# Optimization experiments

Measured on AMD Instinct MI355X. Metric: run time of the kernel, lower is better.

The kernel has to match this reference:

```python
import jax, jax.numpy as jnp
import numpy as np

G, B, I, H = 512, 64, 32, 64  # num_of_grids, batch, input_size, hidden_size


def setup_inputs() -> dict:
    key = jax.random.key(0)
    ks = jax.random.split(key, 13)
    s = lambda *sh: 1.0 / np.sqrt(sh[-1])
    return {
        "input_data": jax.random.normal(ks[0], (G, B, I), jnp.float32),
        "h0": jax.random.normal(ks[1], (B, H), jnp.float32),
        "c0": jax.random.normal(ks[2], (B, H), jnp.float32),
        # LSTMCell params (torch layout: gates ordered i, f, g, o)
        "W_ih": jax.random.uniform(ks[3], (4 * H, I), jnp.float32, -s(H), s(H)),
        "W_hh": jax.random.uniform(ks[4], (4 * H, H), jnp.float32, -s(H), s(H)),
        "b_ih": jax.random.uniform(ks[5], (4 * H,), jnp.float32, -s(H), s(H)),
        "b_hh": jax.random.uniform(ks[6], (4 * H,), jnp.float32, -s(H), s(H)),
        # MLP head: H*G -> 10*G -> 5*G -> G
        "W1": jax.random.uniform(ks[7], (10 * G, H * G), jnp.float32, -s(H * G), s(H * G)),
        "b1": jax.random.uniform(ks[8], (10 * G,), jnp.float32, -s(H * G), s(H * G)),
        "W2": jax.random.uniform(ks[9], (5 * G, 10 * G), jnp.float32, -s(10 * G), s(10 * G)),
        "b2": jax.random.uniform(ks[10], (5 * G,), jnp.float32, -s(10 * G), s(10 * G)),
        "W3": jax.random.uniform(ks[11], (G, 5 * G), jnp.float32, -s(5 * G), s(5 * G)),
        "b3": jax.random.uniform(ks[12], (G,), jnp.float32, -s(5 * G), s(5 * G)),
    }


def reference(input_data, h0, c0, W_ih, W_hh, b_ih, b_hh, W1, b1, W2, b2, W3, b3):
    def step(carry, x):
        h, c = carry
        gates = x @ W_ih.T + b_ih + h @ W_hh.T + b_hh  # [B, 4H]
        i, f, g, o = jnp.split(gates, 4, axis=-1)
        i, f, o = jax.nn.sigmoid(i), jax.nn.sigmoid(f), jax.nn.sigmoid(o)
        g = jnp.tanh(g)
        c = f * c + i * g
        h = o * jnp.tanh(c)
        return (h, c), h

    _, hs = jax.lax.scan(step, (h0, c0), input_data)  # [G, B, H]
    # torch.cat(list, dim=1) over grid order -> [B, G*H]
    out_all = jnp.transpose(hs, (1, 0, 2)).reshape(h0.shape[0], -1)
    x = out_all @ W1.T + b1
    x = x @ W2.T + b2
    x = x @ W3.T + b3
    return jax.nn.sigmoid(x)  # [B, G]
```

## Files before the change

kernel.cpp:

```cpp
#include <hip/hip_runtime.h>
#include <hip/hip_fp16.h>

#define G_ 512
#define B_ 64
#define I_ 32
#define H_ 64
#define NGATE 256

typedef _Float16 half8 __attribute__((ext_vector_type(8)));
typedef _Float16 h4 __attribute__((ext_vector_type(4)));
typedef _Float16 h2 __attribute__((ext_vector_type(2)));
typedef float f32x4 __attribute__((ext_vector_type(4)));

#if __has_builtin(__builtin_amdgcn_fdot2)
#define FDOT2(a, b, c) __builtin_amdgcn_fdot2((a), (b), (c), false)
#else
#define FDOT2(a, b, c) ((c) + (float)(a)[0] * (float)(b)[0] + (float)(a)[1] * (float)(b)[1])
#endif

__device__ __forceinline__ float sigf(float x) {
  return 1.0f / (1.0f + __expf(-x));
}
__device__ __forceinline__ float tanh_fast(float x) {
  x = fminf(fmaxf(x, -15.0f), 15.0f);
  float e = __expf(2.0f * x);
  return (e - 1.0f) / (e + 1.0f);
}

__device__ __forceinline__ void gload_lds16(const _Float16* g, _Float16* l) {
  __builtin_amdgcn_global_load_lds(
      (const __attribute__((address_space(1))) void*)g,
      (__attribute__((address_space(3))) void*)l, 16, 0, 0);
}

__global__ __launch_bounds__(256) void k_xproj(
    const float* __restrict__ input, const float* __restrict__ W_ih,
    const float* __restrict__ b_ih, const float* __restrict__ b_hh,
    _Float16* __restrict__ xproj) {
  const int g = blockIdx.x;
  const int t = threadIdx.x;
  const int col = t >> 2;
  const int q = t & 3;
  const int row = q * H_ + col;
  __shared__ alignas(16) float inp[B_ * I_];
  const float* ing = input + (size_t)g * (B_ * I_);
#pragma unroll
  for (int u = 0; u < (B_ * I_) / 256; ++u) inp[u * 256 + t] = ing[u * 256 + t];
  float w[I_];
#pragma unroll
  for (int k = 0; k < I_; k += 4) {
    f32x4 v = *(const f32x4*)(W_ih + (size_t)row * I_ + k);
    w[k] = v[0]; w[k + 1] = v[1]; w[k + 2] = v[2]; w[k + 3] = v[3];
  }
  const float bias = b_ih[row] + b_hh[row];
  __syncthreads();
  for (int b = 0; b < B_; ++b) {
    float a0 = bias, a1 = 0.f, a2 = 0.f, a3 = 0.f;
#pragma unroll
    for (int k = 0; k < I_; k += 4) {
      f32x4 iv = *(const f32x4*)&inp[b * I_ + k];
      a0 += iv[0] * w[k]; a1 += iv[1] * w[k + 1];
      a2 += iv[2] * w[k + 2]; a3 += iv[3] * w[k + 3];
    }
    xproj[((size_t)b * G_ + g) * NGATE + t] = (_Float16)((a0 + a1) + (a2 + a3));
  }
}

__device__ __forceinline__ void scan_row(
    int b, int j, const _Float16* __restrict__ xproj,
    const float* __restrict__ h0, const float* __restrict__ c0,
    const float* __restrict__ W_hh, _Float16* __restrict__ hs,
    _Float16* hsh) {
  h2 w[4][32];
#pragma unroll
  for (int q = 0; q < 4; ++q) {
    const f32x4* wr = (const f32x4*)(W_hh + (size_t)(q * H_ + j) * H_);
#pragma unroll
    for (int kk = 0; kk < 16; ++kk) {
      f32x4 v = wr[kk];
      h2 t0, t1;
      t0[0] = (_Float16)v[0]; t0[1] = (_Float16)v[1];
      t1[0] = (_Float16)v[2]; t1[1] = (_Float16)v[3];
      w[q][2 * kk] = t0;
      w[q][2 * kk + 1] = t1;
    }
  }
  float c = c0[b * H_ + j];
  hsh[j] = (_Float16)h0[b * H_ + j];

  const h4* xrow = (const h4*)(xproj + (size_t)b * G_ * NGATE) + j;
  h4 p[8];
#pragma unroll
  for (int d = 0; d < 8; ++d) p[d] = xrow[(size_t)d * 64];

  _Float16* hrow = hs + (size_t)b * (G_ * H_) + j;

  for (int g0 = 0; g0 < G_; g0 += 8) {
#pragma unroll
    for (int d = 0; d < 8; ++d) {
      const int g = g0 + d;
      float a[4], a2[4];
#pragma unroll
      for (int q = 0; q < 4; ++q) { a[q] = (float)p[d][q]; a2[q] = 0.0f; }
      const f32x4* hp4 = (const f32x4*)hsh;
#pragma unroll
      for (int k4 = 0; k4 < 4; ++k4) {
        f32x4 hv4 = hp4[k4];
#pragma unroll
        for (int t = 0; t < 4; ++t) {
          h2 hv = __builtin_bit_cast(h2, hv4[t]);
#pragma unroll
          for (int q = 0; q < 4; ++q) a[q] = FDOT2(hv, w[q][k4 * 4 + t], a[q]);
        }
      }
#pragma unroll
      for (int k4 = 4; k4 < 8; ++k4) {
        f32x4 hv4 = hp4[k4];
#pragma unroll
        for (int t = 0; t < 4; ++t) {
          h2 hv = __builtin_bit_cast(h2, hv4[t]);
#pragma unroll
          for (int q = 0; q < 4; ++q) a2[q] = FDOT2(hv, w[q][k4 * 4 + t], a2[q]);
        }
      }
#pragma unroll
      for (int q = 0; q < 4; ++q) a[q] += a2[q];

      float ig = sigf(a[0]);
      float fg = sigf(a[1]);
      float gg = tanh_fast(a[2]);
      float og = sigf(a[3]);
      c = fg * c + ig * gg;
      float hh = og * tanh_fast(c);
      _Float16 hf = (_Float16)hh;
      hsh[j] = hf;
      hrow[(size_t)g * H_] = hf;
      if (g + 8 < G_) p[d] = xrow[(size_t)(g + 8) * 64];
    }
  }
}

template <int N, int K>
__device__ __forceinline__ void conv_tiled(
    const float* __restrict__ src, _Float16* __restrict__ dst,
    int gtid, int gstride) {
  constexpr int KWT = 64;
  constexpr int TILEH = 64 * KWT;
  for (int i = gtid; i < N * (K / 8); i += gstride) {
    const int n = i / (K / 8);
    const int k8 = i % (K / 8);
    const f32x4* s = (const f32x4*)(src + (size_t)n * K + (size_t)k8 * 8);
    f32x4 v0 = s[0];
    f32x4 v1 = s[1];
    half8 h;
    h[0] = (_Float16)v0[0]; h[1] = (_Float16)v0[1];
    h[2] = (_Float16)v0[2]; h[3] = (_Float16)v0[3];
    h[4] = (_Float16)v1[0]; h[5] = (_Float16)v1[1];
    h[6] = (_Float16)v1[2]; h[7] = (_Float16)v1[3];
    const int nt = n >> 6, rr = n & 63;
    const int ksg = k8 >> 3;
    const int kk8 = k8 & 7;
    const size_t tile_id = (size_t)nt * (K / KWT) + ksg;
    int byte = rr * (KWT * 2) + ((kk8 * 16) ^ ((rr & 7) << 4));
    *(half8*)((char*)(dst + tile_id * TILEH) + byte) = h;
  }
}

#define NCONV 2048

__global__ __launch_bounds__(256) void k_scan_conv(
    const _Float16* __restrict__ xproj, const float* __restrict__ h0,
    const float* __restrict__ c0, const float* __restrict__ W_hh,
    _Float16* __restrict__ hs,
    const float* __restrict__ W1, _Float16* __restrict__ W1h,
    const float* __restrict__ W2, _Float16* __restrict__ W2h,
    const float* __restrict__ W3, _Float16* __restrict__ W3h) {
  __shared__ alignas(16) _Float16 hsh[H_];
  const int bid = blockIdx.x;
  if (bid < B_) {
    if (threadIdx.x < 64)
      scan_row(bid, threadIdx.x, xproj, h0, c0, W_hh, hs, hsh);
    return;
  }
  const int gtid = (bid - B_) * 256 + threadIdx.x;
  const int gstride = NCONV * 256;
  conv_tiled<5120, 32768>(W1, W1h, gtid, gstride);
  conv_tiled<2560, 5120>(W2, W2h, gtid, gstride);
  conv_tiled<512, 2560>(W3, W3h, gtid, gstride);
}

template <int N, int K, int KC, int NTILES, int KSPLIT>
__global__ __launch_bounds__(256, 2) void k_gemm_p(
    const _Float16* __restrict__ X, const _Float16* __restrict__ Wh,
    float* __restrict__ part) {
  constexpr int KW = 64;
  constexpr int TILEH = 64 * KW;
  constexpr int CALLS = 8;
  constexpr int NST = KC / KW;
  static_assert(KC % KW == 0 && N == NTILES * 256, "geometry");
  __shared__ alignas(16) _Float16 wl[2][4][TILEH];
  const int bid = blockIdx.x;
  const int nt = bid % NTILES;
  const int ks = bid / NTILES;
  const int n0 = nt * 256;
  const int kbeg = ks * KC;
  const int lane = threadIdx.x & 63;
  const int wave = threadIdx.x >> 6;
  const int r = lane & 15;
  const int gq = lane >> 4;

  const _Float16* tslice = Wh +
      ((size_t)(n0 / 64 + wave) * (K / KW) + (size_t)(kbeg / KW)) * TILEH +
      (size_t)lane * 8;
  _Float16* lbase0 = &wl[0][wave][0];
  _Float16* lbase1 = &wl[1][wave][0];
  const _Float16* xrow = X + (size_t)r * K + kbeg + 8 * gq;

  f32x4 acc[4][4] = {};

#pragma unroll
  for (int c = 0; c < CALLS; ++c)
    gload_lds16(tslice + c * 512, lbase0 + c * 512);

  for (int st = 0; st < NST; ++st) {
    half8 areg[2][4];
#pragma unroll
    for (int k32 = 0; k32 < 2; ++k32)
#pragma unroll
      for (int mi = 0; mi < 4; ++mi)
        areg[k32][mi] =
            *(const half8*)(xrow + st * KW + k32 * 32 + (size_t)(mi * 16) * K);
    __builtin_amdgcn_sched_barrier(0);
    if (st + 1 < NST) {
      const _Float16* tn = tslice + (size_t)(st + 1) * TILEH;
      _Float16* ln = ((st + 1) & 1) ? lbase1 : lbase0;
#pragma unroll
      for (int c = 0; c < CALLS; ++c)
        gload_lds16(tn + c * 512, ln + c * 512);
      __builtin_amdgcn_sched_barrier(0);
      asm volatile("s_waitcnt vmcnt(%0)" ::"i"(CALLS) : "memory");
    } else {
      asm volatile("s_waitcnt vmcnt(0)" ::: "memory");
    }
    __builtin_amdgcn_sched_barrier(0);
    const char* lcur = (const char*)((st & 1) ? lbase1 : lbase0);
#pragma unroll
    for (int k32 = 0; k32 < 2; ++k32) {
#pragma unroll
      for (int ni = 0; ni < 4; ++ni) {
        const int rr = ni * 16 + r;
        int rbyte = rr * (KW * 2) + (((k32 * 32 + 8 * gq) * 2) ^ ((r & 7) << 4));
        half8 bfv = *(const half8*)(lcur + rbyte);
#pragma unroll
        for (int mi = 0; mi < 4; ++mi)
          acc[mi][ni] = __builtin_amdgcn_mfma_f32_16x16x32_f16(
              areg[k32][mi], bfv, acc[mi][ni], 0, 0, 0);
      }
    }
  }
#pragma unroll
  for (int mi = 0; mi < 4; ++mi) {
#pragma unroll
    for (int ni = 0; ni < 4; ++ni) {
#pragma unroll
      for (int q = 0; q < 4; ++q) {
        int row = mi * 16 + gq * 4 + q;
        int col = n0 + wave * 64 + ni * 16 + r;
        part[((size_t)ks * 64 + row) * N + col] = acc[mi][ni][q];
      }
    }
  }
}

template <int N, int KS>
__global__ __launch_bounds__(256) void k_reduce(
    const float* __restrict__ part, const float* __restrict__ bias,
    _Float16* __restrict__ out) {
  const int idx4 = (blockIdx.x * 256 + threadIdx.x) * 4;
  const int n = idx4 % N;
  f32x4 s = *(const f32x4*)(bias + n);
#pragma unroll
  for (int ks = 0; ks < KS; ++ks) s += *(const f32x4*)(part + (size_t)ks * 64 * N + idx4);
#pragma unroll
  for (int t = 0; t < 4; ++t) out[idx4 + t] = (_Float16)s[t];
}

template <int N, int KS>
__global__ __launch_bounds__(256) void k_reduce_sig(
    const float* __restrict__ part, const float* __restrict__ bias,
    float* __restrict__ out) {
  const int idx4 = (blockIdx.x * 256 + threadIdx.x) * 4;
  const int n = idx4 % N;
  f32x4 s = *(const f32x4*)(bias + n);
#pragma unroll
  for (int ks = 0; ks < KS; ++ks) s += *(const f32x4*)(part + (size_t)ks * 64 * N + idx4);
#pragma unroll
  for (int t = 0; t < 4; ++t) out[idx4 + t] = sigf(s[t]);
}

extern "C" void kernel_launch(void* const* d_in, const int* in_sizes, int n_in,
                              void* d_out, int out_size, void* d_ws, size_t ws_size,
                              hipStream_t stream) {
  const float* input = (const float*)d_in[0];
  const float* h0    = (const float*)d_in[1];
  const float* c0    = (const float*)d_in[2];
  const float* W_ih  = (const float*)d_in[3];
  const float* W_hh  = (const float*)d_in[4];
  const float* b_ih  = (const float*)d_in[5];
  const float* b_hh  = (const float*)d_in[6];
  const float* W1    = (const float*)d_in[7];
  const float* b1    = (const float*)d_in[8];
  const float* W2    = (const float*)d_in[9];
  const float* b2    = (const float*)d_in[10];
  const float* W3    = (const float*)d_in[11];
  const float* b3    = (const float*)d_in[12];
  float* out = (float*)d_out;

  uint8_t* ws = (uint8_t*)d_ws;
  float*    part  = (float*)ws;
  _Float16* xproj = (_Float16*)ws;
  _Float16* hs    = (_Float16*)(ws + 41943040);
  _Float16* x2    = (_Float16*)(ws + 46137344);
  _Float16* x3    = (_Float16*)(ws + 46792704);
  _Float16* W1h   = (_Float16*)(ws + 47120384);
  _Float16* W2h   = (_Float16*)(ws + 382664704);
  _Float16* W3h   = (_Float16*)(ws + 408879104);

  k_xproj<<<G_, 256, 0, stream>>>(input, W_ih, b_ih, b_hh, xproj);
  k_scan_conv<<<B_ + NCONV, 256, 0, stream>>>(xproj, h0, c0, W_hh, hs,
                                              W1, W1h, W2, W2h, W3, W3h);
  k_gemm_p<5120, 32768, 1024, 20, 32><<<20 * 32, 256, 0, stream>>>(hs, W1h, part);
  k_reduce<5120, 32><<<(64 * 5120) / 4 / 256, 256, 0, stream>>>(part, b1, x2);
  k_gemm_p<2560, 5120, 320, 10, 16><<<10 * 16, 256, 0, stream>>>(x2, W2h, part);
  k_reduce<2560, 16><<<(64 * 2560) / 4 / 256, 256, 0, stream>>>(part, b2, x3);
  k_gemm_p<512, 2560, 256, 2, 10><<<2 * 10, 256, 0, stream>>>(x3, W3h, part);
  k_reduce_sig<512, 10><<<(64 * 512) / 4 / 256, 256, 0, stream>>>(part, b3, out);
}
```

Before: 415.1 us.

## Split LSTM scan in two phases and overlap tail with first GEMM

The serial LSTM scan is split at grid step 384. The first 384 steps run alongside the weight fp16 conversion. The remaining steps run in a second kernel that also computes the W1 GEMM partials for K-slices covering already-finished timesteps (24 of 32). The leftover 8 K-slices run in a separate GEMM launch. This hides part of the latency-bound scan behind the large first GEMM, at the cost of carrying cell state through global memory, adding one launch, and rearranging the workspace so part no longer aliases xproj.

```diff
diff --git a/kernel.cpp b/kernel.cpp
--- a/kernel.cpp
+++ b/kernel.cpp
@@ -6,6 +6,7 @@
 #define I_ 32
 #define H_ 64
 #define NGATE 256
+#define GSPLIT 384
 
 typedef _Float16 half8 __attribute__((ext_vector_type(8)));
 typedef _Float16 h4 __attribute__((ext_vector_type(4)));
@@ -66,11 +67,12 @@
   }
 }
 
-__device__ __forceinline__ void scan_row(
+template <int GB, int GE, bool FIRST>
+__device__ __forceinline__ void scan_range(
     int b, int j, const _Float16* __restrict__ xproj,
     const float* __restrict__ h0, const float* __restrict__ c0,
-    const float* __restrict__ W_hh, _Float16* __restrict__ hs,
-    _Float16* hsh) {
+    float* __restrict__ cstate, const float* __restrict__ W_hh,
+    _Float16* __restrict__ hs, _Float16* hsh) {
   h2 w[4][32];
 #pragma unroll
   for (int q = 0; q < 4; ++q) {
@@ -85,17 +87,23 @@
       w[q][2 * kk + 1] = t1;
     }
   }
-  float c = c0[b * H_ + j];
-  hsh[j] = (_Float16)h0[b * H_ + j];
+  float c;
+  if (FIRST) {
+    c = c0[b * H_ + j];
+    hsh[j] = (_Float16)h0[b * H_ + j];
+  } else {
+    c = cstate[b * H_ + j];
+    hsh[j] = hs[(size_t)b * (G_ * H_) + (size_t)(GB - 1) * H_ + j];
+  }
 
   const h4* xrow = (const h4*)(xproj + (size_t)b * G_ * NGATE) + j;
   h4 p[8];
 #pragma unroll
-  for (int d = 0; d < 8; ++d) p[d] = xrow[(size_t)d * 64];
+  for (int d = 0; d < 8; ++d) p[d] = xrow[(size_t)(GB + d) * 64];
 
   _Float16* hrow = hs + (size_t)b * (G_ * H_) + j;
 
-  for (int g0 = 0; g0 < G_; g0 += 8) {
+  for (int g0 = GB; g0 < GE; g0 += 8) {
 #pragma unroll
     for (int d = 0; d < 8; ++d) {
       const int g = g0 + d;
@@ -138,6 +146,7 @@
       if (g + 8 < G_) p[d] = xrow[(size_t)(g + 8) * 64];
     }
   }
+  if (FIRST) cstate[b * H_ + j] = c;
 }
 
 template <int N, int K>
@@ -168,10 +177,90 @@
 
 #define NCONV 2048
 
-__global__ __launch_bounds__(256) void k_scan_conv(
+template <int N, int K, int KC>
+__device__ __forceinline__ void gemm_core(
+    int nt, int ks, const _Float16* __restrict__ X,
+    const _Float16* __restrict__ Wh, float* __restrict__ part,
+    _Float16* wl, int tid) {
+  constexpr int KW = 64;
+  constexpr int TILEH = 64 * KW;
+  constexpr int CALLS = 8;
+  constexpr int NST = KC / KW;
+  static_assert(KC % KW == 0, "geometry");
+  const int n0 = nt * 256;
+  const int kbeg = ks * KC;
+  const int lane = tid & 63;
+  const int wave = tid >> 6;
+  const int r = lane & 15;
+  const int gq = lane >> 4;
+
+  const _Float16* tslice = Wh +
+      ((size_t)(n0 / 64 + wave) * (K / KW) + (size_t)(kbeg / KW)) * TILEH +
+      (size_t)lane * 8;
+  _Float16* lbase0 = wl + (size_t)wave * TILEH;
+  _Float16* lbase1 = wl + (size_t)(4 + wave) * TILEH;
+  const _Float16* xrow = X + (size_t)r * K + kbeg + 8 * gq;
+
+  f32x4 acc[4][4] = {};
+
+#pragma unroll
+  for (int c = 0; c < CALLS; ++c)
+    gload_lds16(tslice + c * 512, lbase0 + c * 512);
+
+  for (int st = 0; st < NST; ++st) {
+    half8 areg[2][4];
+#pragma unroll
+    for (int k32 = 0; k32 < 2; ++k32)
+#pragma unroll
+      for (int mi = 0; mi < 4; ++mi)
+        areg[k32][mi] =
+            *(const half8*)(xrow + st * KW + k32 * 32 + (size_t)(mi * 16) * K);
+    __builtin_amdgcn_sched_barrier(0);
+    if (st + 1 < NST) {
+      const _Float16* tn = tslice + (size_t)(st + 1) * TILEH;
+      _Float16* ln = ((st + 1) & 1) ? lbase1 : lbase0;
+#pragma unroll
+      for (int c = 0; c < CALLS; ++c)
+        gload_lds16(tn + c * 512, ln + c * 512);
+      __builtin_amdgcn_sched_barrier(0);
+      asm volatile("s_waitcnt vmcnt(%0)" ::"i"(CALLS) : "memory");
+    } else {
+      asm volatile("s_waitcnt vmcnt(0)" ::: "memory");
+    }
+    __builtin_amdgcn_sched_barrier(0);
+    const char* lcur = (const char*)((st & 1) ? lbase1 : lbase0);
+#pragma unroll
+    for (int k32 = 0; k32 < 2; ++k32) {
+#pragma unroll
+      for (int ni = 0; ni < 4; ++ni) {
+        const int rr = ni * 16 + r;
+        int rbyte = rr * (KW * 2) + (((k32 * 32 + 8 * gq) * 2) ^ ((r & 7) << 4));
+        half8 bfv = *(const half8*)(lcur + rbyte);
+#pragma unroll
+        for (int mi = 0; mi < 4; ++mi)
+          acc[mi][ni] = __builtin_amdgcn_mfma_f32_16x16x32_f16(
+              areg[k32][mi], bfv, acc[mi][ni], 0, 0, 0);
+      }
+    }
+  }
+#pragma unroll
+  for (int mi = 0; mi < 4; ++mi) {
+#pragma unroll
+    for (int ni = 0; ni < 4; ++ni) {
+#pragma unroll
+      for (int q = 0; q < 4; ++q) {
+        int row = mi * 16 + gq * 4 + q;
+        int col = n0 + wave * 64 + ni * 16 + r;
+        part[((size_t)ks * 64 + row) * N + col] = acc[mi][ni][q];
+      }
+    }
+  }
+}
+
+__global__ __launch_bounds__(256) void k_phaseA(
     const _Float16* __restrict__ xproj, const float* __restrict__ h0,
-    const float* __restrict__ c0, const float* __restrict__ W_hh,
-    _Float16* __restrict__ hs,
+    const float* __restrict__ c0, float* __restrict__ cstate,
+    const float* __restrict__ W_hh, _Float16* __restrict__ hs,
     const float* __restrict__ W1, _Float16* __restrict__ W1h,
     const float* __restrict__ W2, _Float16* __restrict__ W2h,
     const float* __restrict__ W3, _Float16* __restrict__ W3h) {
@@ -179,7 +268,8 @@
   const int bid = blockIdx.x;
   if (bid < B_) {
     if (threadIdx.x < 64)
-      scan_row(bid, threadIdx.x, xproj, h0, c0, W_hh, hs, hsh);
+      scan_range<0, GSPLIT, true>(bid, threadIdx.x, xproj, h0, c0, cstate,
+                                  W_hh, hs, hsh);
     return;
   }
   const int gtid = (bid - B_) * 256 + threadIdx.x;
@@ -189,87 +279,34 @@
   conv_tiled<512, 2560>(W3, W3h, gtid, gstride);
 }
 
-template <int N, int K, int KC, int NTILES, int KSPLIT>
+__global__ __launch_bounds__(256, 2) void k_phaseB(
+    const _Float16* __restrict__ xproj, const float* __restrict__ h0,
+    const float* __restrict__ c0, float* __restrict__ cstate,
+    const float* __restrict__ W_hh, _Float16* __restrict__ hs,
+    const _Float16* __restrict__ W1h, float* __restrict__ part) {
+  __shared__ alignas(16) _Float16 wl[8 * 64 * 64];
+  __shared__ alignas(16) _Float16 hsh[H_];
+  const int bid = blockIdx.x;
+  if (bid < B_) {
+    if (threadIdx.x < 64)
+      scan_range<GSPLIT, G_, false>(bid, threadIdx.x, xproj, h0, c0, cstate,
+                                    W_hh, hs, hsh);
+    return;
+  }
+  const int b2 = bid - B_;
+  gemm_core<5120, 32768, 1024>(b2 % 20, b2 / 20, hs, W1h, part, wl,
+                               threadIdx.x);
+}
+
+template <int N, int K, int KC, int NTILES>
 __global__ __launch_bounds__(256, 2) void k_gemm_p(
     const _Float16* __restrict__ X, const _Float16* __restrict__ Wh,
-    float* __restrict__ part) {
-  constexpr int KW = 64;
-  constexpr int TILEH = 64 * KW;
-  constexpr int CALLS = 8;
-  constexpr int NST = KC / KW;
-  static_assert(KC % KW == 0 && N == NTILES * 256, "geometry");
-  __shared__ alignas(16) _Float16 wl[2][4][TILEH];
+    float* __restrict__ part, int ks_off) {
+  static_assert(N == NTILES * 256, "geometry");
+  __shared__ alignas(16) _Float16 wl[8 * 64 * 64];
   const int bid = blockIdx.x;
-  const int nt = bid % NTILES;
-  const int ks = bid / NTILES;
-  const int n0 = nt * 256;
-  const int kbeg = ks * KC;
-  const int lane = threadIdx.x & 63;
-  const int wave = threadIdx.x >> 6;
-  const int r = lane & 15;
-  const int gq = lane >> 4;
-
-  const _Float16* tslice = Wh +
-      ((size_t)(n0 / 64 + wave) * (K / KW) + (size_t)(kbeg / KW)) * TILEH +
-      (size_t)lane * 8;
-  _Float16* lbase0 = &wl[0][wave][0];
-  _Float16* lbase1 = &wl[1][wave][0];
-  const _Float16* xrow = X + (size_t)r * K + kbeg + 8 * gq;
-
-  f32x4 acc[4][4] = {};
-
-#pragma unroll
-  for (int c = 0; c < CALLS; ++c)
-    gload_lds16(tslice + c * 512, lbase0 + c * 512);
-
-  for (int st = 0; st < NST; ++st) {
-    half8 areg[2][4];
-#pragma unroll
-    for (int k32 = 0; k32 < 2; ++k32)
-#pragma unroll
-      for (int mi = 0; mi < 4; ++mi)
-        areg[k32][mi] =
-            *(const half8*)(xrow + st * KW + k32 * 32 + (size_t)(mi * 16) * K);
-    __builtin_amdgcn_sched_barrier(0);
-    if (st + 1 < NST) {
-      const _Float16* tn = tslice + (size_t)(st + 1) * TILEH;
-      _Float16* ln = ((st + 1) & 1) ? lbase1 : lbase0;
-#pragma unroll
-      for (int c = 0; c < CALLS; ++c)
-        gload_lds16(tn + c * 512, ln + c * 512);
-      __builtin_amdgcn_sched_barrier(0);
-      asm volatile("s_waitcnt vmcnt(%0)" ::"i"(CALLS) : "memory");
-    } else {
-      asm volatile("s_waitcnt vmcnt(0)" ::: "memory");
-    }
-    __builtin_amdgcn_sched_barrier(0);
-    const char* lcur = (const char*)((st & 1) ? lbase1 : lbase0);
-#pragma unroll
-    for (int k32 = 0; k32 < 2; ++k32) {
-#pragma unroll
-      for (int ni = 0; ni < 4; ++ni) {
-        const int rr = ni * 16 + r;
-        int rbyte = rr * (KW * 2) + (((k32 * 32 + 8 * gq) * 2) ^ ((r & 7) << 4));
-        half8 bfv = *(const half8*)(lcur + rbyte);
-#pragma unroll
-        for (int mi = 0; mi < 4; ++mi)
-          acc[mi][ni] = __builtin_amdgcn_mfma_f32_16x16x32_f16(
-              areg[k32][mi], bfv, acc[mi][ni], 0, 0, 0);
-      }
-    }
-  }
-#pragma unroll
-  for (int mi = 0; mi < 4; ++mi) {
-#pragma unroll
-    for (int ni = 0; ni < 4; ++ni) {
-#pragma unroll
-      for (int q = 0; q < 4; ++q) {
-        int row = mi * 16 + gq * 4 + q;
-        int col = n0 + wave * 64 + ni * 16 + r;
-        part[((size_t)ks * 64 + row) * N + col] = acc[mi][ni][q];
-      }
-    }
-  }
+  gemm_core<N, K, KC>(bid % NTILES, bid / NTILES + ks_off, X, Wh, part, wl,
+                      threadIdx.x);
 }
 
 template <int N, int KS>
@@ -317,22 +354,25 @@
   float* out = (float*)d_out;
 
   uint8_t* ws = (uint8_t*)d_ws;
-  float*    part  = (float*)ws;
-  _Float16* xproj = (_Float16*)ws;
-  _Float16* hs    = (_Float16*)(ws + 41943040);
-  _Float16* x2    = (_Float16*)(ws + 46137344);
-  _Float16* x3    = (_Float16*)(ws + 46792704);
-  _Float16* W1h   = (_Float16*)(ws + 47120384);
-  _Float16* W2h   = (_Float16*)(ws + 382664704);
-  _Float16* W3h   = (_Float16*)(ws + 408879104);
+  _Float16* xproj  = (_Float16*)ws;
+  _Float16* hs     = (_Float16*)(ws + 16777216);
+  _Float16* x2     = (_Float16*)(ws + 20971520);
+  _Float16* x3     = (_Float16*)(ws + 21626880);
+  float*    cstate = (float*)(ws + 21954560);
+  float*    part   = (float*)(ws + 22020096);
+  _Float16* W1h    = (_Float16*)(ws + 67108864);
+  _Float16* W2h    = (_Float16*)(ws + 402653184);
+  _Float16* W3h    = (_Float16*)(ws + 428867584);
 
   k_xproj<<<G_, 256, 0, stream>>>(input, W_ih, b_ih, b_hh, xproj);
-  k_scan_conv<<<B_ + NCONV, 256, 0, stream>>>(xproj, h0, c0, W_hh, hs,
-                                              W1, W1h, W2, W2h, W3, W3h);
-  k_gemm_p<5120, 32768, 1024, 20, 32><<<20 * 32, 256, 0, stream>>>(hs, W1h, part);
+  k_phaseA<<<B_ + NCONV, 256, 0, stream>>>(xproj, h0, c0, cstate, W_hh, hs,
+                                           W1, W1h, W2, W2h, W3, W3h);
+  k_phaseB<<<B_ + 20 * 24, 256, 0, stream>>>(xproj, h0, c0, cstate, W_hh, hs,
+                                             W1h, part);
+  k_gemm_p<5120, 32768, 1024, 20><<<20 * 8, 256, 0, stream>>>(hs, W1h, part, 24);
   k_reduce<5120, 32><<<(64 * 5120) / 4 / 256, 256, 0, stream>>>(part, b1, x2);
-  k_gemm_p<2560, 5120, 320, 10, 16><<<10 * 16, 256, 0, stream>>>(x2, W2h, part);
+  k_gemm_p<2560, 5120, 320, 10><<<10 * 16, 256, 0, stream>>>(x2, W2h, part, 0);
   k_reduce<2560, 16><<<(64 * 2560) / 4 / 256, 256, 0, stream>>>(part, b2, x3);
-  k_gemm_p<512, 2560, 256, 2, 10><<<2 * 10, 256, 0, stream>>>(x3, W3h, part);
+  k_gemm_p<512, 2560, 256, 2><<<2 * 10, 256, 0, stream>>>(x3, W3h, part, 0);
   k_reduce_sig<512, 10><<<(64 * 512) / 4 / 256, 256, 0, stream>>>(part, b3, out);
 }
```

After: 434.9 us. +4.8%, slower.
